# Kernel optimization log

Measured on AMD Instinct MI355X. Metric: run time of the kernel, lower is better.

## Reference

```python
import jax, jax.numpy as jnp
import numpy as np

N, IN_DIM, E, EDGE_DIM = 50000, 128, 600000, 16
D, H, L = 128, 4, 2
C = D // H  # 32
NEG_SLOPE = 0.2
EPS = 1e-5


def setup_inputs() -> dict:
    key = jax.random.key(0)
    ks = jax.random.split(key, 20)
    x = jax.random.normal(ks[0], (N, IN_DIM), dtype=jnp.float32)
    src = jax.random.randint(ks[1], (E,), 0, N)
    dst = jax.random.randint(ks[2], (E,), 0, N)
    src = jnp.where(src == dst, (src + 1) % N, src)  # no pre-existing self loops
    edge_index = jnp.stack([src, dst]).astype(jnp.int64)
    edge_attr = jax.random.normal(ks[3], (E, EDGE_DIM), dtype=jnp.float32)
    s = 0.05
    p = {
        'in_w': jax.random.normal(ks[4], (IN_DIM, D)) * s,
        'in_b': jnp.zeros((D,), jnp.float32),
        'Wl': jax.random.normal(ks[5], (L, D, D)) * s,
        'bl': jnp.zeros((L, D), jnp.float32),
        'Wr': jax.random.normal(ks[6], (L, D, D)) * s,
        'br': jnp.zeros((L, D), jnp.float32),
        'We': jax.random.normal(ks[7], (L, EDGE_DIM, D)) * s,
        'att': jax.random.normal(ks[8], (L, H, C)) * s,
        'cb': jnp.zeros((L, D), jnp.float32),
        'ln_g': jnp.ones((D,), jnp.float32),
        'ln_b': jnp.zeros((D,), jnp.float32),
        'h1w': jax.random.normal(ks[9], (D, D // 2)) * s,
        'h1b': jnp.zeros((D // 2,), jnp.float32),
        'h2w': jax.random.normal(ks[10], (D // 2, 3)) * s,
        'h2b': jnp.zeros((3,), jnp.float32),
    }
    return {'x': x, 'edge_index': edge_index, 'edge_attr': edge_attr, **p}


def _forward(x, edge_attr, in_w, in_b, Wl, bl, Wr, br, We, att, cb,
             ln_g, ln_b, h1w, h1b, h2w, h2b, src0, dst0):
    n = x.shape[0]
    # add_self_loops with fill_value='mean': loop edge_attr = mean of incoming edge_attr per node
    deg = jax.ops.segment_sum(jnp.ones_like(dst0, dtype=x.dtype), dst0, n)
    loop_attr = jax.ops.segment_sum(edge_attr, dst0, n) / jnp.maximum(deg, 1.0)[:, None]
    idx = jnp.arange(n, dtype=src0.dtype)
    src = jnp.concatenate([src0, idx])
    dst = jnp.concatenate([dst0, idx])
    ea = jnp.concatenate([edge_attr, loop_attr])  # [E+N, EDGE_DIM]

    h = x @ in_w + in_b  # [N, D]
    for l in range(L):
        xl = (h @ Wl[l] + bl[l]).reshape(n, H, C)
        xr = (h @ Wr[l] + br[l]).reshape(n, H, C)
        ee = (ea @ We[l]).reshape(-1, H, C)
        m = xl[src] + xr[dst] + ee                      # [E', H, C]
        m = jnp.where(m > 0, m, NEG_SLOPE * m)          # LeakyReLU(0.2)
        logit = jnp.einsum('ehc,hc->eh', m, att[l])     # [E', H]
        mx = jax.ops.segment_max(logit, dst, n)         # every node has a self loop -> finite
        a = jnp.exp(logit - mx[dst])
        den = jax.ops.segment_sum(a, dst, n)
        a = a / den[dst]                                # scatter softmax over destinations
        out = jax.ops.segment_sum(a[..., None] * xl[src], dst, n)  # [N, H, C]
        h = jax.nn.elu(out.reshape(n, D) + cb[l])       # conv bias then ELU (dropout=eval)
    mu = jnp.mean(h, axis=-1, keepdims=True)
    var = jnp.mean((h - mu) ** 2, axis=-1, keepdims=True)
    h = (h - mu) * jax.lax.rsqrt(var + EPS) * ln_g + ln_b
    h = jax.nn.relu(h @ h1w + h1b)
    return h @ h2w + h2b  # [N, 3]


def reference(x, edge_index, edge_attr, in_w, in_b, Wl, bl, Wr, br, We, att, cb,
              ln_g, ln_b, h1w, h1b, h2w, h2b):
    return _forward(x, edge_attr, in_w, in_b, Wl, bl, Wr, br, We, att, cb,
                    ln_g, ln_b, h1w, h1b, h2w, h2b, edge_index[0], edge_index[1])
```

## Files before the change

### kernel.cpp

```cpp
#include <hip/hip_runtime.h>

#define NEG_SLOPE 0.2f
#define LN_EPS 1e-5f

typedef float f2 __attribute__((ext_vector_type(2)));
typedef short s16x8 __attribute__((ext_vector_type(8)));
typedef float f32x4 __attribute__((ext_vector_type(4)));

__device__ __forceinline__ f2 sp2(float x){ return (f2){x, x}; }
__device__ __forceinline__ f2 fma2(f2 a, f2 b, f2 c){
#if __has_builtin(__builtin_elementwise_fma)
  return __builtin_elementwise_fma(a, b, c);
#else
  f2 r; r.x = fmaf(a.x, b.x, c.x); r.y = fmaf(a.y, b.y, c.y); return r;
#endif
}
__device__ __forceinline__ f2 max2(f2 a, f2 b){
#if __has_builtin(__builtin_elementwise_max)
  return __builtin_elementwise_max(a, b);
#else
  f2 r; r.x = fmaxf(a.x, b.x); r.y = fmaxf(a.y, b.y); return r;
#endif
}
__device__ __forceinline__ f2 min2(f2 a, f2 b){
#if __has_builtin(__builtin_elementwise_min)
  return __builtin_elementwise_min(a, b);
#else
  f2 r; r.x = fminf(a.x, b.x); r.y = fminf(a.y, b.y); return r;
#endif
}
__device__ __forceinline__ float wsum64(float v){
  #pragma unroll
  for (int o = 32; o >= 1; o >>= 1) v += __shfl_xor(v, o);
  return v;
}
__device__ __forceinline__ unsigned short f2b(float f){
  unsigned u = __float_as_uint(f);
  return (unsigned short)((u + 0x7fffu + ((u >> 16) & 1u)) >> 16);
}

__global__ void k_count(const int* __restrict__ dst, int* __restrict__ deg, int E){
  int e = blockIdx.x * blockDim.x + threadIdx.x;
  if (e < E) atomicAdd(&deg[dst[e]], 1);
}

__global__ void k_scan_blk(const int* __restrict__ deg, int* __restrict__ part,
                           int* __restrict__ sums, int n){
  __shared__ int buf[256];
  int t = threadIdx.x, i = blockIdx.x * 256 + t;
  int v = (i < n) ? deg[i] : 0;
  buf[t] = v; __syncthreads();
  #pragma unroll
  for (int off = 1; off < 256; off <<= 1){
    int x = (t >= off) ? buf[t - off] : 0;
    __syncthreads(); buf[t] += x; __syncthreads();
  }
  if (i < n) part[i] = buf[t] - v;
  if (t == 255) sums[blockIdx.x] = buf[255];
}

__global__ void k_scan_top(int* __restrict__ sums, int nb){
  __shared__ int buf[256];
  int t = threadIdx.x;
  int v = (t < nb) ? sums[t] : 0;
  buf[t] = v; __syncthreads();
  #pragma unroll
  for (int off = 1; off < 256; off <<= 1){
    int x = (t >= off) ? buf[t - off] : 0;
    __syncthreads(); buf[t] += x; __syncthreads();
  }
  if (t < nb) sums[t] = buf[t] - v;
}

__global__ void k_scan_add(int* __restrict__ ptr, const int* __restrict__ sums,
                           int n, int Etot){
  int i = blockIdx.x * 256 + threadIdx.x;
  if (i < n) ptr[i] += sums[blockIdx.x];
  if (i == 0) ptr[n] = Etot;
}

__global__ void k_fill(const int* __restrict__ dst, const int* __restrict__ src,
                       int* __restrict__ cnt, const int* __restrict__ ptr,
                       const float* __restrict__ ea, float* __restrict__ cea,
                       int* __restrict__ sx, int E){
  int e = blockIdx.x * blockDim.x + threadIdx.x;
  if (e < E){
    int d = dst[e];
    int pos = atomicAdd(&cnt[d], 1);
    int p = ptr[d] + pos;
    sx[p] = src[e];
    const float4* s4 = (const float4*)(ea + (size_t)e * 16);
    float4* d4 = (float4*)(cea + (size_t)p * 16);
    d4[0] = s4[0]; d4[1] = s4[1]; d4[2] = s4[2]; d4[3] = s4[3];
  }
}

__global__ void k_cvt(const float* __restrict__ X, unsigned short* __restrict__ Xb,
                      long n4){
  long i = (long)blockIdx.x * blockDim.x + threadIdx.x;
  long i4 = i * 4;
  if (i4 < n4){
    float4 v = *(const float4*)(X + i4);
    ushort4 o; o.x = f2b(v.x); o.y = f2b(v.y); o.z = f2b(v.z); o.w = f2b(v.w);
    *(ushort4*)(Xb + i4) = o;
  }
}

__global__ void k_pack(const float* __restrict__ w0, const float* __restrict__ w1,
                       const float* __restrict__ w2, const float* __restrict__ w3,
                       const float* __restrict__ w4, unsigned short* __restrict__ Bp){
  int id = blockIdx.x * blockDim.x + threadIdx.x;
  if (id >= 5 * 2048) return;
  int mat = id >> 11, rem = id & 2047;
  int c = rem >> 8, q = (rem >> 6) & 3, l = rem & 63;
  const float* W = mat == 0 ? w0 : mat == 1 ? w1 : mat == 2 ? w2 : mat == 3 ? w3 : w4;
  unsigned short* o = Bp + ((size_t)mat * 2048 + rem) * 8;
  int kb = q * 32 + (l >> 4) * 8;
  int col = c * 16 + (l & 15);
  #pragma unroll
  for (int j = 0; j < 8; j++) o[j] = f2b(W[(kb + j) * 128 + col]);
}

__launch_bounds__(256)
__global__ void k_mm(const unsigned short* __restrict__ A,
                     const unsigned short* __restrict__ Bp,
                     const float* __restrict__ bias,
                     unsigned short* __restrict__ Yb, int M){
  const int ln = threadIdx.x & 63;
  const int rowBase = (blockIdx.x * 4 + (threadIdx.x >> 6)) * 16;
  const int r16 = ln & 15, quad = ln >> 4;
  int row = rowBase + r16; if (row >= M) row = M - 1;
  const unsigned short* ap = A + (size_t)row * 128 + quad * 8;
  s16x8 af[4];
  #pragma unroll
  for (int q = 0; q < 4; q++) af[q] = *(const s16x8*)(ap + q * 32);
  f32x4 acc[8];
  #pragma unroll
  for (int c = 0; c < 8; c++){
    acc[c] = (f32x4){0.f, 0.f, 0.f, 0.f};
    #pragma unroll
    for (int q = 0; q < 4; q++){
      s16x8 bf = *(const s16x8*)(Bp + ((size_t)(c * 4 + q) * 64 + ln) * 8);
      acc[c] = __builtin_amdgcn_mfma_f32_16x16x32_bf16(af[q], bf, acc[c], 0, 0, 0);
    }
  }
  #pragma unroll
  for (int c = 0; c < 8; c++){
    int col = c * 16 + r16;
    float bv = bias[col];
    #pragma unroll
    for (int r = 0; r < 4; r++){
      int orow = rowBase + quad * 4 + r;
      if (orow < M) Yb[(size_t)orow * 128 + col] = f2b(acc[c][r] + bv);
    }
  }
}

__launch_bounds__(256)
__global__ void k_mm_lr(const unsigned short* __restrict__ A,
                        const unsigned short* __restrict__ BpL,
                        const unsigned short* __restrict__ BpR,
                        const float* __restrict__ bL, const float* __restrict__ bR,
                        float* __restrict__ YL, float* __restrict__ YR, int M){
  const int ln = threadIdx.x & 63;
  const int rowBase = (blockIdx.x * 4 + (threadIdx.x >> 6)) * 16;
  const int r16 = ln & 15, quad = ln >> 4;
  int row = rowBase + r16; if (row >= M) row = M - 1;
  const unsigned short* ap = A + (size_t)row * 128 + quad * 8;
  s16x8 af[4];
  #pragma unroll
  for (int q = 0; q < 4; q++) af[q] = *(const s16x8*)(ap + q * 32);
  f32x4 aL[8], aR[8];
  #pragma unroll
  for (int c = 0; c < 8; c++){
    aL[c] = (f32x4){0.f, 0.f, 0.f, 0.f};
    aR[c] = (f32x4){0.f, 0.f, 0.f, 0.f};
    #pragma unroll
    for (int q = 0; q < 4; q++){
      s16x8 bfl = *(const s16x8*)(BpL + ((size_t)(c * 4 + q) * 64 + ln) * 8);
      s16x8 bfr = *(const s16x8*)(BpR + ((size_t)(c * 4 + q) * 64 + ln) * 8);
      aL[c] = __builtin_amdgcn_mfma_f32_16x16x32_bf16(af[q], bfl, aL[c], 0, 0, 0);
      aR[c] = __builtin_amdgcn_mfma_f32_16x16x32_bf16(af[q], bfr, aR[c], 0, 0, 0);
    }
  }
  #pragma unroll
  for (int c = 0; c < 8; c++){
    int col = c * 16 + r16;
    float bvl = bL[col], bvr = bR[col];
    #pragma unroll
    for (int r = 0; r < 4; r++){
      int orow = rowBase + quad * 4 + r;
      if (orow < M){
        YL[(size_t)orow * 128 + col] = aL[c][r] + bvl;
        YR[(size_t)orow * 128 + col] = aR[c][r] + bvr;
      }
    }
  }
}

__launch_bounds__(256)
__global__ void k_gat(const float* __restrict__ xl, const float* __restrict__ xr,
                      const float* __restrict__ cea, const int* __restrict__ sx,
                      const int* __restrict__ ptr,
                      const float* __restrict__ We, const float* __restrict__ att,
                      const float* __restrict__ cbv,
                      float* __restrict__ hf, unsigned short* __restrict__ hb,
                      int N, int E, int wf, int wb){
  __shared__ float4 sea4[4][4][64];
  const int t = threadIdx.x & 63;
  const int wv = threadIdx.x >> 6;
  const int c0 = 2 * t;

  f2 we[16];
  #pragma unroll
  for (int k = 0; k < 16; k++) we[k] = *(const f2*)(We + k * 128 + c0);
  const f2 atv = *(const f2*)(att + c0);
  const f2 cbf = *(const f2*)(cbv + c0);

  for (int n = blockIdx.x * 4 + wv; n < N; n += gridDim.x * 4){
    const int beg = __builtin_amdgcn_readfirstlane(ptr[n]);
    const int end = __builtin_amdgcn_readfirstlane(ptr[n + 1]);
    const int deg = end - beg;

    const f2 xrv = *(const f2*)(xr + (size_t)n * 128 + c0);
    const f2 xln = *(const f2*)(xl + (size_t)n * 128 + c0);

    f2 acc = sp2(0.f), eesum = sp2(0.f);
    float den = 0.f;

    for (int cbase = beg; cbase < end; cbase += 64){
      const int cn = __builtin_amdgcn_readfirstlane(min(64, end - cbase));
      int sv = (t < cn) ? sx[cbase + t] : 0;
      const bool st = (t < cn);
      const float4* sp4 = (const float4*)(cea + (size_t)(cbase + (st ? t : 0)) * 16);
      float4 r0 = sp4[0], r1 = sp4[1], r2 = sp4[2], r3 = sp4[3];

      f2 xs[16];
      auto issueA = [&](int sub){
        #pragma unroll
        for (int i = 0; i < 16; i++){
          int s = __builtin_amdgcn_readlane(sv, sub + i);
          xs[i] = *(const f2*)(xl + (size_t)s * 128 + c0);
        }
      };
      auto phaseB = [&](int sub){
        #pragma unroll
        for (int i = 0; i < 16; i++){
          const int item = sub + i;
          const float vm = (item < cn) ? 1.f : 0.f;
          const int it = (item < cn) ? item : 0;
          float4 a0 = sea4[wv][0][it];
          float4 a1 = sea4[wv][1][it];
          float4 a2 = sea4[wv][2][it];
          float4 a3 = sea4[wv][3][it];
          f2 e0, e1;
          e0 = sp2(a0.x) * we[0];
          e0 = fma2(sp2(a0.y), we[1],  e0);
          e0 = fma2(sp2(a0.z), we[2],  e0);
          e0 = fma2(sp2(a0.w), we[3],  e0);
          e0 = fma2(sp2(a1.x), we[4],  e0);
          e0 = fma2(sp2(a1.y), we[5],  e0);
          e0 = fma2(sp2(a1.z), we[6],  e0);
          e0 = fma2(sp2(a1.w), we[7],  e0);
          e1 = sp2(a2.x) * we[8];
          e1 = fma2(sp2(a2.y), we[9],  e1);
          e1 = fma2(sp2(a2.z), we[10], e1);
          e1 = fma2(sp2(a2.w), we[11], e1);
          e1 = fma2(sp2(a3.x), we[12], e1);
          e1 = fma2(sp2(a3.y), we[13], e1);
          e1 = fma2(sp2(a3.z), we[14], e1);
          e1 = fma2(sp2(a3.w), we[15], e1);
          f2 ee = e0 + e1;
          eesum = fma2(sp2(vm), ee, eesum);
          f2 m = xs[i] + xrv + ee;
          m = fma2(sp2(NEG_SLOPE), min2(m, sp2(0.f)), max2(m, sp2(0.f)));
          f2 pr = m * atv;
          float pl = pr.x + pr.y;
          pl += __shfl_xor(pl, 1); pl += __shfl_xor(pl, 2);
          pl += __shfl_xor(pl, 4); pl += __shfl_xor(pl, 8);
          float p = __expf(pl) * vm;
          den += p;
          acc = fma2(sp2(p), xs[i], acc);
        }
      };

      issueA(0);
      if (st){
        sea4[wv][0][t] = r0; sea4[wv][1][t] = r1;
        sea4[wv][2][t] = r2; sea4[wv][3][t] = r3;
      }
      phaseB(0);
      for (int sub = 16; sub < cn; sub += 16){
        issueA(sub);
        phaseB(sub);
      }
    }

    {
      float rdeg = 1.f / fmaxf((float)deg, 1.f);
      f2 m = xln + xrv + eesum * sp2(rdeg);
      m = fma2(sp2(NEG_SLOPE), min2(m, sp2(0.f)), max2(m, sp2(0.f)));
      f2 pr = m * atv;
      float pl = pr.x + pr.y;
      pl += __shfl_xor(pl, 1); pl += __shfl_xor(pl, 2);
      pl += __shfl_xor(pl, 4); pl += __shfl_xor(pl, 8);
      float p = __expf(pl);
      den += p;
      acc = fma2(sp2(p), xln, acc);
    }

    float rd = 1.f / den;
    f2 o = fma2(acc, sp2(rd), cbf);
    float o0 = o.x > 0.f ? o.x : expm1f(o.x);
    float o1 = o.y > 0.f ? o.y : expm1f(o.y);
    if (wf) *(f2*)(hf + (size_t)n * 128 + c0) = (f2){o0, o1};
    if (wb){
      unsigned packed = (unsigned)f2b(o0) | ((unsigned)f2b(o1) << 16);
      *(unsigned*)(hb + (size_t)n * 128 + c0) = packed;
    }
  }
}

__launch_bounds__(256)
__global__ void k_head(const float* __restrict__ h, const float* __restrict__ g,
                       const float* __restrict__ b, const float* __restrict__ w1,
                       const float* __restrict__ b1, const float* __restrict__ w2,
                       const float* __restrict__ b2, float* __restrict__ out, int N){
  __shared__ float sn[4][128];
  const int t = threadIdx.x & 63, wv = threadIdx.x >> 6;
  for (int node = blockIdx.x * 4 + wv; node < N; node += gridDim.x * 4){
    float h0 = h[(size_t)node * 128 + t];
    float h1 = h[(size_t)node * 128 + 64 + t];
    float mu = wsum64(h0 + h1) * (1.f / 128.f);
    float d0 = h0 - mu, d1 = h1 - mu;
    float var = wsum64(d0 * d0 + d1 * d1) * (1.f / 128.f);
    float rstd = rsqrtf(var + LN_EPS);
    sn[wv][t]      = d0 * rstd * g[t]      + b[t];
    sn[wv][t + 64] = d1 * rstd * g[t + 64] + b[t + 64];
    float a = b1[t];
    #pragma unroll
    for (int k4 = 0; k4 < 32; k4++){
      float4 v = *(const float4*)&sn[wv][k4 * 4];
      a = fmaf(v.x, w1[(k4 * 4 + 0) * 64 + t], a);
      a = fmaf(v.y, w1[(k4 * 4 + 1) * 64 + t], a);
      a = fmaf(v.z, w1[(k4 * 4 + 2) * 64 + t], a);
      a = fmaf(v.w, w1[(k4 * 4 + 3) * 64 + t], a);
    }
    a = fmaxf(a, 0.f);
    float p0 = a * w2[t * 3 + 0], p1 = a * w2[t * 3 + 1], p2 = a * w2[t * 3 + 2];
    p0 = wsum64(p0); p1 = wsum64(p1); p2 = wsum64(p2);
    if (t == 0){
      out[(size_t)node * 3 + 0] = p0 + b2[0];
      out[(size_t)node * 3 + 1] = p1 + b2[1];
      out[(size_t)node * 3 + 2] = p2 + b2[2];
    }
  }
}

extern "C" void kernel_launch(void* const* d_in, const int* in_sizes, int n_in,
                              void* d_out, int out_size, void* d_ws, size_t ws_size,
                              hipStream_t stream){
  const float* x    = (const float*)d_in[0];
  const int*   ei   = (const int*)d_in[1];
  const float* ea   = (const float*)d_in[2];
  const float* in_w = (const float*)d_in[3];
  const float* in_b = (const float*)d_in[4];
  const float* Wl   = (const float*)d_in[5];
  const float* bl   = (const float*)d_in[6];
  const float* Wr   = (const float*)d_in[7];
  const float* br   = (const float*)d_in[8];
  const float* We   = (const float*)d_in[9];
  const float* att  = (const float*)d_in[10];
  const float* cb   = (const float*)d_in[11];
  const float* lng  = (const float*)d_in[12];
  const float* lnb  = (const float*)d_in[13];
  const float* h1w  = (const float*)d_in[14];
  const float* h1b  = (const float*)d_in[15];
  const float* h2w  = (const float*)d_in[16];
  const float* h2b  = (const float*)d_in[17];
  float* out = (float*)d_out;

  int N = in_sizes[0] / 128;
  int E = in_sizes[1] / 2;
  const int* src = ei;
  const int* dst = ei + E;

  char* w = (char*)d_ws;
  size_t off = 0;
  auto alloc = [&](size_t bytes) -> char* {
    char* p = w + off;
    off = (off + bytes + 255) & ~(size_t)255;
    return p;
  };
  int*   deg   = (int*)alloc((size_t)N * 4);
  int*   cnt   = (int*)alloc((size_t)N * 4);
  int*   ptr   = (int*)alloc((size_t)(N + 1) * 4);
  int*   bsum  = (int*)alloc(256 * 4);
  int*   sx    = (int*)alloc((size_t)E * 4);
  float* cea   = (float*)alloc((size_t)E * 16 * 4);
  unsigned short* xb    = (unsigned short*)alloc((size_t)N * 128 * 2);
  unsigned short* hb_in = (unsigned short*)alloc((size_t)N * 128 * 2);
  unsigned short* Bp    = (unsigned short*)alloc((size_t)5 * 16384 * 2);
  float* hf    = (float*)alloc((size_t)N * 128 * 4);
  float* xlb   = (float*)alloc((size_t)N * 128 * 4);
  float* xrb   = (float*)alloc((size_t)N * 128 * 4);

  int nb = (N + 255) / 256;
  hipMemsetAsync(deg, 0, (size_t)N * 4, stream);
  hipMemsetAsync(cnt, 0, (size_t)N * 4, stream);
  k_count<<<(E + 255) / 256, 256, 0, stream>>>(dst, deg, E);
  k_scan_blk<<<nb, 256, 0, stream>>>(deg, ptr, bsum, N);
  k_scan_top<<<1, 256, 0, stream>>>(bsum, nb);
  k_scan_add<<<nb, 256, 0, stream>>>(ptr, bsum, N, E);
  k_fill<<<(E + 255) / 256, 256, 0, stream>>>(dst, src, cnt, ptr, ea, cea, sx, E);

  long n4 = (long)N * 128;
  k_cvt<<<(int)((n4 / 4 + 255) / 256), 256, 0, stream>>>(x, xb, n4);
  k_pack<<<(5 * 2048 + 255) / 256, 256, 0, stream>>>(in_w, Wl, Wl + 16384, Wr, Wr + 16384, Bp);

  int gblocks = (N + 63) / 64;
  int nodeBlocks = (N + 3) / 4;
  int gatBlocks = nodeBlocks < 2048 ? nodeBlocks : 2048;
  k_mm<<<gblocks, 256, 0, stream>>>(xb, Bp, in_b, hb_in, N);
  for (int l = 0; l < 2; l++){
    const unsigned short* Ain = (l == 0) ? hb_in : xb;
    k_mm_lr<<<gblocks, 256, 0, stream>>>(Ain, Bp + (size_t)(1 + l) * 16384,
                                         Bp + (size_t)(3 + l) * 16384,
                                         bl + l * 128, br + l * 128, xlb, xrb, N);
    k_gat<<<gatBlocks, 256, 0, stream>>>(xlb, xrb, cea, sx, ptr,
                                         We + l * 2048, att + l * 128, cb + l * 128,
                                         hf, xb, N, E, (l == 1) ? 1 : 0, (l == 0) ? 1 : 0);
  }
  k_head<<<gatBlocks, 256, 0, stream>>>(hf, lng, lnb, h1w, h1b, h2w, h2b, out, N);
}
```

Measured before the change: 548.0 us.

## Compute GAT edge embeddings with bf16 MFMA and store edge attrs as bf16

The per-edge projection edge_attr @ We is moved from scalar packed-FMA loops to 16x16x32 bf16 MFMA tiles, with We pre-packed into MFMA B-fragment layout and K zero-padded from 16 to 32. Results go through a per-wave LDS tile that each lane then reads. The CSR-sorted edge attributes are stored as bf16, halving their footprint and read traffic. The earlier overlap of LDS staging with gathers is dropped, and edge features lose precision to bf16. Half of each MFMA's K dimension is wasted on padding.

```diff
diff --git a/kernel.cpp b/kernel.cpp
--- a/kernel.cpp
+++ b/kernel.cpp
@@ -4,6 +4,7 @@
 #define LN_EPS 1e-5f
 
 typedef float f2 __attribute__((ext_vector_type(2)));
+typedef short s16x4 __attribute__((ext_vector_type(4)));
 typedef short s16x8 __attribute__((ext_vector_type(8)));
 typedef float f32x4 __attribute__((ext_vector_type(4)));
 
@@ -81,7 +82,7 @@
 
 __global__ void k_fill(const int* __restrict__ dst, const int* __restrict__ src,
                        int* __restrict__ cnt, const int* __restrict__ ptr,
-                       const float* __restrict__ ea, float* __restrict__ cea,
+                       const float* __restrict__ ea, unsigned short* __restrict__ ceab,
                        int* __restrict__ sx, int E){
   int e = blockIdx.x * blockDim.x + threadIdx.x;
   if (e < E){
@@ -90,8 +91,13 @@
     int p = ptr[d] + pos;
     sx[p] = src[e];
     const float4* s4 = (const float4*)(ea + (size_t)e * 16);
-    float4* d4 = (float4*)(cea + (size_t)p * 16);
-    d4[0] = s4[0]; d4[1] = s4[1]; d4[2] = s4[2]; d4[3] = s4[3];
+    float4 a0 = s4[0], a1 = s4[1], a2 = s4[2], a3 = s4[3];
+    ushort4 o0 = {f2b(a0.x), f2b(a0.y), f2b(a0.z), f2b(a0.w)};
+    ushort4 o1 = {f2b(a1.x), f2b(a1.y), f2b(a1.z), f2b(a1.w)};
+    ushort4 o2 = {f2b(a2.x), f2b(a2.y), f2b(a2.z), f2b(a2.w)};
+    ushort4 o3 = {f2b(a3.x), f2b(a3.y), f2b(a3.z), f2b(a3.w)};
+    ushort4* d4 = (ushort4*)(ceab + (size_t)p * 16);
+    d4[0] = o0; d4[1] = o1; d4[2] = o2; d4[3] = o3;
   }
 }
 
@@ -119,6 +125,21 @@
   int col = c * 16 + (l & 15);
   #pragma unroll
   for (int j = 0; j < 8; j++) o[j] = f2b(W[(kb + j) * 128 + col]);
+}
+
+__global__ void k_packwe(const float* __restrict__ We, unsigned short* __restrict__ Bpwe){
+  int id = blockIdx.x * blockDim.x + threadIdx.x;
+  if (id >= 2 * 8 * 64) return;
+  int layer = id >> 9, rem = id & 511, c = rem >> 6, l = rem & 63;
+  const float* W = We + (size_t)layer * 2048;
+  unsigned short* o = Bpwe + (size_t)id * 8;
+  int kb = (l >> 4) * 8;
+  int col = c * 16 + (l & 15);
+  #pragma unroll
+  for (int j = 0; j < 8; j++){
+    int k = kb + j;
+    o[j] = (k < 16) ? f2b(W[k * 128 + col]) : (unsigned short)0;
+  }
 }
 
 __launch_bounds__(256)
@@ -200,22 +221,25 @@
 
 __launch_bounds__(256)
 __global__ void k_gat(const float* __restrict__ xl, const float* __restrict__ xr,
-                      const float* __restrict__ cea, const int* __restrict__ sx,
-                      const int* __restrict__ ptr,
-                      const float* __restrict__ We, const float* __restrict__ att,
-                      const float* __restrict__ cbv,
+                      const unsigned short* __restrict__ ceab,
+                      const int* __restrict__ sx, const int* __restrict__ ptr,
+                      const unsigned short* __restrict__ Bpwe,
+                      const float* __restrict__ att, const float* __restrict__ cbv,
                       float* __restrict__ hf, unsigned short* __restrict__ hb,
-                      int N, int E, int wf, int wb){
-  __shared__ float4 sea4[4][4][64];
+                      int N, int wf, int wb){
+  __shared__ float lee[4][16 * 130];
   const int t = threadIdx.x & 63;
   const int wv = threadIdx.x >> 6;
   const int c0 = 2 * t;
-
-  f2 we[16];
-  #pragma unroll
-  for (int k = 0; k < 16; k++) we[k] = *(const f2*)(We + k * 128 + c0);
+  const int l15 = t & 15, q = t >> 4;
+
+  s16x8 bwe[8];
+  #pragma unroll
+  for (int c = 0; c < 8; c++) bwe[c] = *(const s16x8*)(Bpwe + ((size_t)c * 64 + t) * 8);
   const f2 atv = *(const f2*)(att + c0);
   const f2 cbf = *(const f2*)(cbv + c0);
+  float* lw = &lee[wv][0];
+  const int wbase = q * 4 * 130 + l15;
 
   for (int n = blockIdx.x * 4 + wv; n < N; n += gridDim.x * 4){
     const int beg = __builtin_amdgcn_readfirstlane(ptr[n]);
@@ -231,46 +255,31 @@
     for (int cbase = beg; cbase < end; cbase += 64){
       const int cn = __builtin_amdgcn_readfirstlane(min(64, end - cbase));
       int sv = (t < cn) ? sx[cbase + t] : 0;
-      const bool st = (t < cn);
-      const float4* sp4 = (const float4*)(cea + (size_t)(cbase + (st ? t : 0)) * 16);
-      float4 r0 = sp4[0], r1 = sp4[1], r2 = sp4[2], r3 = sp4[3];
-
-      f2 xs[16];
-      auto issueA = [&](int sub){
+
+      for (int sub = 0; sub < cn; sub += 16){
+        s16x8 af = (s16x8){0, 0, 0, 0, 0, 0, 0, 0};
+        if (q < 2)
+          af = *(const s16x8*)(ceab + (size_t)(cbase + sub + l15) * 16 + q * 8);
+        f2 xs[16];
         #pragma unroll
         for (int i = 0; i < 16; i++){
           int s = __builtin_amdgcn_readlane(sv, sub + i);
           xs[i] = *(const f2*)(xl + (size_t)s * 128 + c0);
         }
-      };
-      auto phaseB = [&](int sub){
+        #pragma unroll
+        for (int c = 0; c < 8; c++){
+          f32x4 ee4 = __builtin_amdgcn_mfma_f32_16x16x32_bf16(
+              af, bwe[c], (f32x4){0.f, 0.f, 0.f, 0.f}, 0, 0, 0);
+          #pragma unroll
+          for (int r = 0; r < 4; r++)
+            lw[wbase + r * 130 + c * 16] = ee4[r];
+        }
         #pragma unroll
         for (int i = 0; i < 16; i++){
           const int item = sub + i;
           const float vm = (item < cn) ? 1.f : 0.f;
-          const int it = (item < cn) ? item : 0;
-          float4 a0 = sea4[wv][0][it];
-          float4 a1 = sea4[wv][1][it];
-          float4 a2 = sea4[wv][2][it];
-          float4 a3 = sea4[wv][3][it];
-          f2 e0, e1;
-          e0 = sp2(a0.x) * we[0];
-          e0 = fma2(sp2(a0.y), we[1],  e0);
-          e0 = fma2(sp2(a0.z), we[2],  e0);
-          e0 = fma2(sp2(a0.w), we[3],  e0);
-          e0 = fma2(sp2(a1.x), we[4],  e0);
-          e0 = fma2(sp2(a1.y), we[5],  e0);
-          e0 = fma2(sp2(a1.z), we[6],  e0);
-          e0 = fma2(sp2(a1.w), we[7],  e0);
-          e1 = sp2(a2.x) * we[8];
-          e1 = fma2(sp2(a2.y), we[9],  e1);
-          e1 = fma2(sp2(a2.z), we[10], e1);
-          e1 = fma2(sp2(a2.w), we[11], e1);
-          e1 = fma2(sp2(a3.x), we[12], e1);
-          e1 = fma2(sp2(a3.y), we[13], e1);
-          e1 = fma2(sp2(a3.z), we[14], e1);
-          e1 = fma2(sp2(a3.w), we[15], e1);
-          f2 ee = e0 + e1;
+          const int it = (item < cn) ? i : 0;
+          f2 ee = *(const f2*)&lw[it * 130 + c0];
           eesum = fma2(sp2(vm), ee, eesum);
           f2 m = xs[i] + xrv + ee;
           m = fma2(sp2(NEG_SLOPE), min2(m, sp2(0.f)), max2(m, sp2(0.f)));
@@ -282,17 +291,6 @@
           den += p;
           acc = fma2(sp2(p), xs[i], acc);
         }
-      };
-
-      issueA(0);
-      if (st){
-        sea4[wv][0][t] = r0; sea4[wv][1][t] = r1;
-        sea4[wv][2][t] = r2; sea4[wv][3][t] = r3;
-      }
-      phaseB(0);
-      for (int sub = 16; sub < cn; sub += 16){
-        issueA(sub);
-        phaseB(sub);
       }
     }
 
@@ -397,10 +395,11 @@
   int*   ptr   = (int*)alloc((size_t)(N + 1) * 4);
   int*   bsum  = (int*)alloc(256 * 4);
   int*   sx    = (int*)alloc((size_t)E * 4);
-  float* cea   = (float*)alloc((size_t)E * 16 * 4);
+  unsigned short* ceab = (unsigned short*)alloc((size_t)(E + 64) * 16 * 2);
   unsigned short* xb    = (unsigned short*)alloc((size_t)N * 128 * 2);
   unsigned short* hb_in = (unsigned short*)alloc((size_t)N * 128 * 2);
   unsigned short* Bp    = (unsigned short*)alloc((size_t)5 * 16384 * 2);
+  unsigned short* Bpwe  = (unsigned short*)alloc((size_t)2 * 4096 * 2);
   float* hf    = (float*)alloc((size_t)N * 128 * 4);
   float* xlb   = (float*)alloc((size_t)N * 128 * 4);
   float* xrb   = (float*)alloc((size_t)N * 128 * 4);
@@ -412,11 +411,12 @@
   k_scan_blk<<<nb, 256, 0, stream>>>(deg, ptr, bsum, N);
   k_scan_top<<<1, 256, 0, stream>>>(bsum, nb);
   k_scan_add<<<nb, 256, 0, stream>>>(ptr, bsum, N, E);
-  k_fill<<<(E + 255) / 256, 256, 0, stream>>>(dst, src, cnt, ptr, ea, cea, sx, E);
+  k_fill<<<(E + 255) / 256, 256, 0, stream>>>(dst, src, cnt, ptr, ea, ceab, sx, E);
 
   long n4 = (long)N * 128;
   k_cvt<<<(int)((n4 / 4 + 255) / 256), 256, 0, stream>>>(x, xb, n4);
   k_pack<<<(5 * 2048 + 255) / 256, 256, 0, stream>>>(in_w, Wl, Wl + 16384, Wr, Wr + 16384, Bp);
+  k_packwe<<<4, 256, 0, stream>>>(We, Bpwe);
 
   int gblocks = (N + 63) / 64;
   int nodeBlocks = (N + 3) / 4;
@@ -427,9 +427,10 @@
     k_mm_lr<<<gblocks, 256, 0, stream>>>(Ain, Bp + (size_t)(1 + l) * 16384,
                                          Bp + (size_t)(3 + l) * 16384,
                                          bl + l * 128, br + l * 128, xlb, xrb, N);
-    k_gat<<<gatBlocks, 256, 0, stream>>>(xlb, xrb, cea, sx, ptr,
-                                         We + l * 2048, att + l * 128, cb + l * 128,
-                                         hf, xb, N, E, (l == 1) ? 1 : 0, (l == 0) ? 1 : 0);
+    k_gat<<<gatBlocks, 256, 0, stream>>>(xlb, xrb, ceab, sx, ptr,
+                                         Bpwe + (size_t)l * 4096,
+                                         att + l * 128, cb + l * 128,
+                                         hf, xb, N, (l == 1) ? 1 : 0, (l == 0) ? 1 : 0);
   }
   k_head<<<gatBlocks, 256, 0, stream>>>(hf, lng, lnb, h1w, h1b, h2w, h2b, out, N);
 }
```

New measurement: 507.6 us. 1.08x faster.
